# Performance work log

Hardware: AMD Instinct MI355X
Metric: run time of the kernel (lower is better)

## Reference

```python
import jax, jax.numpy as jnp
import numpy as np

K = 5        # kernel_size
F0 = 3       # features[0]
F1 = 3       # features[1]
N = 2097152  # ring length (number of sites)
NOISE = 0.01

# triple_product[a,b,c] = cross(tetra[a], tetra[b]) @ tetra[c], shape (4,4,4)
_t = np.array([[0.0, 0.0, 1.0],
               [(8/9)**0.5, 0.0, -1/3],
               [-(2/9)**0.5, (2/3)**0.5, -1/3],
               [-(2/9)**0.5, -(2/3)**0.5, -1/3]], dtype=np.float64)
_cross = np.cross(_t[:, None, :], _t[None, :, :])          # (4,4,3)
TRIPLE_PRODUCT = jnp.asarray(np.einsum('abd,cd->abc', _cross, _t), dtype=jnp.float32)


def setup_inputs() -> dict:
    key = jax.random.key(0)
    ks = jax.random.split(key, 5)
    x = jax.random.randint(ks[0], (N,), 0, 4, dtype=jnp.int32)
    input_kernel_dot = NOISE * jax.random.normal(ks[1], (F0, K), jnp.float32)
    input_kernel_triple = NOISE * jax.random.normal(ks[2], (F0, K, K), jnp.float32)
    kernel_0 = jax.random.normal(ks[3], (K, 2 * F0, F1), jnp.float32) / np.float32(np.sqrt(K * 2 * F0))
    bias_0 = jnp.zeros((1, F1), jnp.float32)
    dense_w = jax.random.normal(ks[4], (F1, 1), jnp.float32) / np.float32(np.sqrt(F1))
    return {"x": x, "input_kernel_dot": input_kernel_dot,
            "input_kernel_triple": input_kernel_triple, "kernel_0": kernel_0,
            "bias_0": bias_0, "dense_w": dense_w}


def reference(x, input_kernel_dot, input_kernel_triple, kernel_0, bias_0, dense_w):
    n = x.shape[0]
    i = jnp.arange(n)
    # ring neighbors x[(i+1)..(i+K) mod N], shape (N, K)
    nbr = (i[:, None] + jnp.arange(1, K + 1)[None, :]) % n
    xn = x[nbr]
    # dot channel: +/-1 same-spin indicator contracted with (F0,K) kernel
    same = 2.0 * (x[:, None] == xn).astype(jnp.float32) - 1.0      # (N,K)
    y_dot = jnp.einsum('fk,nk->nf', input_kernel_dot, same)        # (N,F0)
    # triple channel: antisymmetrized kernel against triple-product lookup
    anti = input_kernel_triple - jnp.swapaxes(input_kernel_triple, 1, 2)   # (F0,K,K)
    tpl = TRIPLE_PRODUCT[x[:, None, None], xn[:, :, None], xn[:, None, :]]  # (N,K,K)
    y_triple = jnp.einsum('fjk,njk->nf', anti, tpl)                # (N,F0)
    y = jax.nn.elu(jnp.concatenate([y_dot, y_triple], axis=1))     # (N,2*F0)
    # circular conv layer: roll(y, i)[:K][j] == y[(j - i) % N]
    conv_idx = (jnp.arange(K)[None, :] - i[:, None]) % n           # (N,K)
    y = jnp.einsum('jcf,njc->nf', kernel_0, y[conv_idx]) + bias_0  # (N,F1)
    y = jax.nn.elu(y)
    y = jnp.mean(y, axis=0)                                        # (F1,)
    return (y @ dense_w).ravel()[0]
```

## Files before the change

### kernel.cpp

```cpp
#include <hip/hip_runtime.h>
#include <math.h>

#define NSITES 2097152
#define NMASK  (NSITES - 1)

typedef _Float16 half2_t __attribute__((ext_vector_type(2)));

__device__ __forceinline__ float elu1(float v) {
    return v > 0.0f ? v : __expf(v) - 1.0f;
}

__device__ __forceinline__ float tp_val(int a, int b, int c) {
    if (a == b || b == c || a == c) return 0.0f;
    int inv = (a > b) + (a > c) + (b > c);
    int d   = 6 - a - b - c;
    float base = (d & 1) ? 0.76980035891950105f : -0.76980035891950105f;
    return (inv & 1) ? -base : base;
}

__global__ __launch_bounds__(1024) void su2_fused_kernel(
    const int*   __restrict__ x,
    const float* __restrict__ kdot,
    const float* __restrict__ ktri,
    const float* __restrict__ k0,
    const float* __restrict__ bias,
    const float* __restrict__ dw,
    float*       __restrict__ out)
{
    __shared__ half2_t      t01[4096];
    __shared__ half2_t      t23[4096];
    __shared__ half2_t      t45[4096];
    __shared__ unsigned int hc[1024];
    __shared__ float        tp[64];
    __shared__ float        red[16];

    const int tid = threadIdx.x;

    const int m0 = (blockIdx.x * 1024 + tid) * 8;
    const int4 xa = *reinterpret_cast<const int4*>(x + m0);
    const int4 xb = *reinterpret_cast<const int4*>(x + m0 + 4);

    int4 e0, e1, e2;
    if (tid >= 1022) {
        e0 = *reinterpret_cast<const int4*>(x + ((m0 + 8)  & NMASK));
        e1 = *reinterpret_cast<const int4*>(x + ((m0 + 12) & NMASK));
        e2 = *reinterpret_cast<const int4*>(x + ((m0 + 16) & NMASK));
    }

    if (tid < 64) tp[tid] = tp_val(tid >> 4, (tid >> 2) & 3, tid & 3);

    unsigned int half =
        (unsigned)xa.x | ((unsigned)xa.y << 2) | ((unsigned)xa.z << 4) | ((unsigned)xa.w << 6) |
        ((unsigned)xb.x << 8) | ((unsigned)xb.y << 10) | ((unsigned)xb.z << 12) | ((unsigned)xb.w << 14);
    hc[tid] = half;

    float kd[3][5];
    #pragma unroll
    for (int f = 0; f < 3; ++f)
        #pragma unroll
        for (int k = 0; k < 5; ++k) kd[f][k] = kdot[f * 5 + k];

    float an[3][10];
    #pragma unroll
    for (int f = 0; f < 3; ++f) {
        int p = 0;
        #pragma unroll
        for (int j = 0; j < 5; ++j)
            #pragma unroll
            for (int k = j + 1; k < 5; ++k) {
                an[f][p] = 2.0f * (ktri[f * 25 + j * 5 + k] - ktri[f * 25 + k * 5 + j]);
                ++p;
            }
    }

    half2_t w01[5][3], w23[5][3], w45[5][3];
    #pragma unroll
    for (int j = 0; j < 5; ++j)
        #pragma unroll
        for (int f = 0; f < 3; ++f) {
            w01[j][f] = half2_t{(_Float16)k0[(j * 6 + 0) * 3 + f], (_Float16)k0[(j * 6 + 1) * 3 + f]};
            w23[j][f] = half2_t{(_Float16)k0[(j * 6 + 2) * 3 + f], (_Float16)k0[(j * 6 + 3) * 3 + f]};
            w45[j][f] = half2_t{(_Float16)k0[(j * 6 + 4) * 3 + f], (_Float16)k0[(j * 6 + 5) * 3 + f]};
        }
    __syncthreads();

    {
        const int a = tid & 3;
        int nb[4];
        #pragma unroll
        for (int k = 0; k < 4; ++k) nb[k] = (tid >> (2 + 2 * k)) & 3;

        float yd0 = 0.f, yd1 = 0.f, yd2 = 0.f;
        #pragma unroll
        for (int k = 0; k < 4; ++k) {
            const float sm = (a == nb[k]) ? 1.0f : -1.0f;
            yd0 = fmaf(kd[0][k], sm, yd0);
            yd1 = fmaf(kd[1][k], sm, yd1);
            yd2 = fmaf(kd[2][k], sm, yd2);
        }

        float ft0 = 0.f, ft1 = 0.f, ft2 = 0.f;
        {
            const int pj[6] = {0, 0, 0, 1, 1, 2};
            const int pk[6] = {1, 2, 3, 2, 3, 3};
            const int pp[6] = {0, 1, 2, 4, 5, 7};
            #pragma unroll
            for (int q = 0; q < 6; ++q) {
                const float t = tp[(a << 4) + (nb[pj[q]] << 2) + nb[pk[q]]];
                ft0 = fmaf(an[0][pp[q]], t, ft0);
                ft1 = fmaf(an[1][pp[q]], t, ft1);
                ft2 = fmaf(an[2][pp[q]], t, ft2);
            }
        }

        #pragma unroll
        for (int i = 0; i < 4; ++i) {
            const int code = tid + 1024 * i;
            const float sm4 = (a == i) ? 1.0f : -1.0f;
            const float d0v = fmaf(kd[0][4], sm4, yd0);
            const float d1v = fmaf(kd[1][4], sm4, yd1);
            const float d2v = fmaf(kd[2][4], sm4, yd2);

            float t0 = ft0, t1 = ft1, t2 = ft2;
            const int p4[4] = {3, 6, 8, 9};
            #pragma unroll
            for (int j = 0; j < 4; ++j) {
                const float t = tp[(a << 4) + (nb[j] << 2) + i];
                t0 = fmaf(an[0][p4[j]], t, t0);
                t1 = fmaf(an[1][p4[j]], t, t1);
                t2 = fmaf(an[2][p4[j]], t, t2);
            }

            t01[code] = half2_t{(_Float16)elu1(d0v), (_Float16)elu1(d1v)};
            t23[code] = half2_t{(_Float16)elu1(d2v), (_Float16)elu1(t0)};
            t45[code] = half2_t{(_Float16)elu1(t1),  (_Float16)elu1(t2)};
        }
    }
    __syncthreads();

    unsigned long long code;
    if (tid < 1022) {
        code = (unsigned long long)half
             | ((unsigned long long)hc[tid + 1] << 16)
             | ((unsigned long long)(hc[tid + 2] & 3u) << 32);
    } else {
        code = (unsigned long long)half
             | ((unsigned long long)(unsigned)e0.x << 16) | ((unsigned long long)(unsigned)e0.y << 18)
             | ((unsigned long long)(unsigned)e0.z << 20) | ((unsigned long long)(unsigned)e0.w << 22)
             | ((unsigned long long)(unsigned)e1.x << 24) | ((unsigned long long)(unsigned)e1.y << 26)
             | ((unsigned long long)(unsigned)e1.z << 28) | ((unsigned long long)(unsigned)e1.w << 30)
             | ((unsigned long long)(unsigned)e2.x << 32);
    }

    const float b0 = bias[0], b1 = bias[1], b2 = bias[2];
    float acc[8][3];
    #pragma unroll
    for (int o = 0; o < 8; ++o) { acc[o][0] = b0; acc[o][1] = b1; acc[o][2] = b2; }

    #pragma unroll
    for (int i = 0; i < 12; ++i) {
        const int idx = (int)((code >> (2 * i)) & 0xFFFull);
        const half2_t v01 = t01[idx];
        const half2_t v23 = t23[idx];
        const half2_t v45 = t45[idx];
        #pragma unroll
        for (int j = 0; j < 5; ++j) {
            const int o = i - j;
            if (o >= 0 && o < 8) {
                #pragma unroll
                for (int f = 0; f < 3; ++f) {
                    float a = acc[o][f];
                    a = __builtin_amdgcn_fdot2(v01, w01[j][f], a, false);
                    a = __builtin_amdgcn_fdot2(v23, w23[j][f], a, false);
                    a = __builtin_amdgcn_fdot2(v45, w45[j][f], a, false);
                    acc[o][f] = a;
                }
            }
        }
    }

    const float d0 = dw[0], d1 = dw[1], d2 = dw[2];
    float partial = 0.0f;
    #pragma unroll
    for (int o = 0; o < 8; ++o)
        partial += elu1(acc[o][0]) * d0 + elu1(acc[o][1]) * d1 + elu1(acc[o][2]) * d2;

    #pragma unroll
    for (int off = 32; off > 0; off >>= 1)
        partial += __shfl_down(partial, off, 64);

    if ((tid & 63) == 0) red[tid >> 6] = partial;
    __syncthreads();

    if (tid == 0) {
        float s = 0.0f;
        #pragma unroll
        for (int w = 0; w < 16; ++w) s += red[w];
        atomicAdd(out, s * (1.0f / (float)NSITES));
    }
}

extern "C" void kernel_launch(void* const* d_in, const int* in_sizes, int n_in,
                              void* d_out, int out_size, void* d_ws, size_t ws_size,
                              hipStream_t stream) {
    const int*   x    = (const int*)  d_in[0];
    const float* kdot = (const float*)d_in[1];
    const float* ktri = (const float*)d_in[2];
    const float* k0   = (const float*)d_in[3];
    const float* bias = (const float*)d_in[4];
    const float* dw   = (const float*)d_in[5];
    float* out = (float*)d_out;

    su2_fused_kernel<<<NSITES / 8192, 1024, 0, stream>>>(x, kdot, ktri, k0, bias, dw, out);
}
```

Before: 80.93 us.

## Halve sites per thread, force uniform conv weights, and target two blocks per CU

Each thread now handles 4 sites instead of 8, so the grid doubles to 512 blocks and the packed neighbour code fits in 32 bits. The conv weights are forced wave-uniform with readfirstlane so they can sit in scalar registers, and launch bounds ask for two 1024-thread blocks per CU. The aim is to lower VGPR pressure and raise occupancy. The trade-off is that every block still rebuilds the 4096-entry lookup table, so the table-building work per site doubles.

New measurement: 85.36 us. 5.5% more time.

```diff
diff --git a/kernel.cpp b/kernel.cpp
--- a/kernel.cpp
+++ b/kernel.cpp
@@ -8,6 +8,12 @@
 
 __device__ __forceinline__ float elu1(float v) {
     return v > 0.0f ? v : __expf(v) - 1.0f;
+}
+
+__device__ __forceinline__ half2_t uni(half2_t v) {
+    int b = __builtin_bit_cast(int, v);
+    b = __builtin_amdgcn_readfirstlane(b);
+    return __builtin_bit_cast(half2_t, b);
 }
 
 __device__ __forceinline__ float tp_val(int a, int b, int c) {
@@ -18,7 +24,7 @@
     return (inv & 1) ? -base : base;
 }
 
-__global__ __launch_bounds__(1024) void su2_fused_kernel(
+__global__ __launch_bounds__(1024, 2) void su2_fused_kernel(
     const int*   __restrict__ x,
     const float* __restrict__ kdot,
     const float* __restrict__ ktri,
@@ -36,23 +42,21 @@
 
     const int tid = threadIdx.x;
 
-    const int m0 = (blockIdx.x * 1024 + tid) * 8;
+    const int m0 = (blockIdx.x * 1024 + tid) * 4;
     const int4 xa = *reinterpret_cast<const int4*>(x + m0);
-    const int4 xb = *reinterpret_cast<const int4*>(x + m0 + 4);
 
     int4 e0, e1, e2;
-    if (tid >= 1022) {
-        e0 = *reinterpret_cast<const int4*>(x + ((m0 + 8)  & NMASK));
-        e1 = *reinterpret_cast<const int4*>(x + ((m0 + 12) & NMASK));
-        e2 = *reinterpret_cast<const int4*>(x + ((m0 + 16) & NMASK));
+    if (tid >= 1021) {
+        e0 = *reinterpret_cast<const int4*>(x + ((m0 + 4)  & NMASK));
+        e1 = *reinterpret_cast<const int4*>(x + ((m0 + 8)  & NMASK));
+        e2 = *reinterpret_cast<const int4*>(x + ((m0 + 12) & NMASK));
     }
 
     if (tid < 64) tp[tid] = tp_val(tid >> 4, (tid >> 2) & 3, tid & 3);
 
-    unsigned int half =
-        (unsigned)xa.x | ((unsigned)xa.y << 2) | ((unsigned)xa.z << 4) | ((unsigned)xa.w << 6) |
-        ((unsigned)xb.x << 8) | ((unsigned)xb.y << 10) | ((unsigned)xb.z << 12) | ((unsigned)xb.w << 14);
-    hc[tid] = half;
+    const unsigned int myhc =
+        (unsigned)xa.x | ((unsigned)xa.y << 2) | ((unsigned)xa.z << 4) | ((unsigned)xa.w << 6);
+    hc[tid] = myhc;
 
     float kd[3][5];
     #pragma unroll
@@ -78,9 +82,9 @@
     for (int j = 0; j < 5; ++j)
         #pragma unroll
         for (int f = 0; f < 3; ++f) {
-            w01[j][f] = half2_t{(_Float16)k0[(j * 6 + 0) * 3 + f], (_Float16)k0[(j * 6 + 1) * 3 + f]};
-            w23[j][f] = half2_t{(_Float16)k0[(j * 6 + 2) * 3 + f], (_Float16)k0[(j * 6 + 3) * 3 + f]};
-            w45[j][f] = half2_t{(_Float16)k0[(j * 6 + 4) * 3 + f], (_Float16)k0[(j * 6 + 5) * 3 + f]};
+            w01[j][f] = uni(half2_t{(_Float16)k0[(j * 6 + 0) * 3 + f], (_Float16)k0[(j * 6 + 1) * 3 + f]});
+            w23[j][f] = uni(half2_t{(_Float16)k0[(j * 6 + 2) * 3 + f], (_Float16)k0[(j * 6 + 3) * 3 + f]});
+            w45[j][f] = uni(half2_t{(_Float16)k0[(j * 6 + 4) * 3 + f], (_Float16)k0[(j * 6 + 5) * 3 + f]});
         }
     __syncthreads();
 
@@ -138,35 +142,31 @@
     }
     __syncthreads();
 
-    unsigned long long code;
-    if (tid < 1022) {
-        code = (unsigned long long)half
-             | ((unsigned long long)hc[tid + 1] << 16)
-             | ((unsigned long long)(hc[tid + 2] & 3u) << 32);
+    unsigned int code;
+    if (tid < 1021) {
+        code = myhc | (hc[tid + 1] << 8) | (hc[tid + 2] << 16) | ((hc[tid + 3] & 3u) << 24);
     } else {
-        code = (unsigned long long)half
-             | ((unsigned long long)(unsigned)e0.x << 16) | ((unsigned long long)(unsigned)e0.y << 18)
-             | ((unsigned long long)(unsigned)e0.z << 20) | ((unsigned long long)(unsigned)e0.w << 22)
-             | ((unsigned long long)(unsigned)e1.x << 24) | ((unsigned long long)(unsigned)e1.y << 26)
-             | ((unsigned long long)(unsigned)e1.z << 28) | ((unsigned long long)(unsigned)e1.w << 30)
-             | ((unsigned long long)(unsigned)e2.x << 32);
+        code = myhc
+             | ((unsigned)e0.x << 8)  | ((unsigned)e0.y << 10) | ((unsigned)e0.z << 12) | ((unsigned)e0.w << 14)
+             | ((unsigned)e1.x << 16) | ((unsigned)e1.y << 18) | ((unsigned)e1.z << 20) | ((unsigned)e1.w << 22)
+             | ((unsigned)e2.x << 24);
     }
 
     const float b0 = bias[0], b1 = bias[1], b2 = bias[2];
-    float acc[8][3];
-    #pragma unroll
-    for (int o = 0; o < 8; ++o) { acc[o][0] = b0; acc[o][1] = b1; acc[o][2] = b2; }
-
-    #pragma unroll
-    for (int i = 0; i < 12; ++i) {
-        const int idx = (int)((code >> (2 * i)) & 0xFFFull);
+    float acc[4][3];
+    #pragma unroll
+    for (int o = 0; o < 4; ++o) { acc[o][0] = b0; acc[o][1] = b1; acc[o][2] = b2; }
+
+    #pragma unroll
+    for (int i = 0; i < 8; ++i) {
+        const int idx = (int)((code >> (2 * i)) & 0xFFFu);
         const half2_t v01 = t01[idx];
         const half2_t v23 = t23[idx];
         const half2_t v45 = t45[idx];
         #pragma unroll
         for (int j = 0; j < 5; ++j) {
             const int o = i - j;
-            if (o >= 0 && o < 8) {
+            if (o >= 0 && o < 4) {
                 #pragma unroll
                 for (int f = 0; f < 3; ++f) {
                     float a = acc[o][f];
@@ -182,7 +182,7 @@
     const float d0 = dw[0], d1 = dw[1], d2 = dw[2];
     float partial = 0.0f;
     #pragma unroll
-    for (int o = 0; o < 8; ++o)
+    for (int o = 0; o < 4; ++o)
         partial += elu1(acc[o][0]) * d0 + elu1(acc[o][1]) * d1 + elu1(acc[o][2]) * d2;
 
     #pragma unroll
@@ -211,5 +211,5 @@
     const float* dw   = (const float*)d_in[5];
     float* out = (float*)d_out;
 
-    su2_fused_kernel<<<NSITES / 8192, 1024, 0, stream>>>(x, kdot, ktri, k0, bias, dw, out);
-}
+    su2_fused_kernel<<<NSITES / 4096, 1024, 0, stream>>>(x, kdot, ktri, k0, bias, dw, out);
+}
```
